# Optimization experiments

Measured on AMD Instinct MI355X. Metric: run time of the kernel, lower is better.

## Reference

```python
import jax, jax.numpy as jnp
import numpy as np
import math

B, L, D, N = 8, 4096, 1024, 16

def setup_inputs() -> dict:
    key = jax.random.key(0)
    k1, k2, k3, k4, k5, k6 = jax.random.split(key, 6)
    return {
        "x": jax.random.normal(k1, (B, L, D), dtype=jnp.float32),
        "delta": jax.random.normal(k2, (D, N, 1), dtype=jnp.float32),
        "alpha": jax.random.normal(k3, (D, N, 1), dtype=jnp.float32),
        "beta": jax.random.normal(k4, (D, N, 1), dtype=jnp.float32),
        "gamma": jax.random.normal(k5, (D, N), dtype=jnp.float32),
        "omega": jax.random.normal(k6, (D,), dtype=jnp.float32),
    }

def reference(x, delta, alpha, beta, gamma, omega):
    # x: (B, L, D). Unidirectional EMA, no state, no padding mask.
    b, l, d = x.shape
    n_state = gamma.shape[-1]
    scale = math.sqrt(1.0 / n_state)

    residual = x * omega  # (B, L, D)
    xt = jnp.swapaxes(x, -1, -2)  # (B, D, L)

    # EMA coefficients
    p = jax.nn.sigmoid(delta)          # (D, N, 1)
    a = jax.nn.sigmoid(alpha)          # (D, N, 1)
    q = 1.0 - p * a                    # (D, N, 1)

    # Vandermonde kernel: k[d, t] = sum_n p*beta*q^t * gamma*scale
    t = jnp.arange(l, dtype=x.dtype)   # (L,)
    vander = t[None, None, :] * jnp.log(q)          # (D, N, L)
    kernel = p * beta * jnp.exp(vander)             # (D, N, L)
    k = jnp.einsum('dnl,dn->dl', kernel, gamma * scale)  # (D, L)

    # FFT long convolution with zero-padding to 2L (linear conv)
    n_fft = 2 * l
    k_f = jnp.fft.rfft(k, n=n_fft)                  # (D, L+1) complex
    x_f = jnp.fft.rfft(xt, n=n_fft)                 # (B, D, L+1) complex
    out = jnp.fft.irfft(x_f * k_f, n=n_fft)[..., :l]  # (B, D, L)

    return jnp.swapaxes(out, -1, -2) + residual     # (B, L, D)
```

## Files before the change

kernel.cpp:

```cpp
#include <hip/hip_runtime.h>

#define BB 8
#define LL 4096
#define DD 1024
#define NN 16
#define GG 32
#define CC (LL / GG)
#define UF 8

__device__ __forceinline__ float sigmoid_precise(float v) {
    return 1.0f / (1.0f + expf(-v));
}

__global__ __launch_bounds__(256) void ema_chunk_states(
    const float* __restrict__ x,
    const float* __restrict__ delta,
    const float* __restrict__ alpha,
    float* __restrict__ E)
{
    const int g = blockIdx.x;
    const int d = blockIdx.y * 256 + threadIdx.x;
    const int b = blockIdx.z;

    float q[NN];
#pragma unroll
    for (int n = 0; n < NN; ++n) {
        float p = sigmoid_precise(delta[d * NN + n]);
        float a = sigmoid_precise(alpha[d * NN + n]);
        q[n] = 1.0f - p * a;
    }

    float u[NN];
#pragma unroll
    for (int n = 0; n < NN; ++n) u[n] = 0.0f;

    const float* xp = x + ((size_t)b * LL + (size_t)g * CC) * DD + d;
    for (int ii = 0; ii < CC; ii += UF) {
        float xv[UF];
#pragma unroll
        for (int j = 0; j < UF; ++j)
            xv[j] = xp[(size_t)(ii + j) * DD];
#pragma unroll
        for (int j = 0; j < UF; ++j) {
#pragma unroll
            for (int n = 0; n < NN; ++n)
                u[n] = fmaf(q[n], u[n], xv[j]);
        }
    }

    float* Ep = E + (((size_t)b * GG + g) * NN) * DD + d;
#pragma unroll
    for (int n = 0; n < NN; ++n)
        Ep[(size_t)n * DD] = u[n];
}

__global__ __launch_bounds__(256) void ema_final(
    const float* __restrict__ x,
    const float* __restrict__ delta,
    const float* __restrict__ alpha,
    const float* __restrict__ beta,
    const float* __restrict__ gamma,
    const float* __restrict__ omega,
    const float* __restrict__ E,
    float* __restrict__ out)
{
    const int g = blockIdx.x;
    const int d = blockIdx.y * 256 + threadIdx.x;
    const int b = blockIdx.z;

    float q[NN], gc[NN];
#pragma unroll
    for (int n = 0; n < NN; ++n) {
        float p = sigmoid_precise(delta[d * NN + n]);
        float a = sigmoid_precise(alpha[d * NN + n]);
        q[n]  = 1.0f - p * a;
        gc[n] = p * beta[d * NN + n] * gamma[d * NN + n] * 0.25f;
    }

    float u[NN];
#pragma unroll
    for (int n = 0; n < NN; ++n) u[n] = 0.0f;
    if (g > 0) {
        float Q[NN];
#pragma unroll
        for (int n = 0; n < NN; ++n) Q[n] = powf(q[n], (float)CC);
        for (int gp = 0; gp < g; ++gp) {
            const float* Ep = E + (((size_t)b * GG + gp) * NN) * DD + d;
#pragma unroll
            for (int n = 0; n < NN; ++n)
                u[n] = fmaf(Q[n], u[n], Ep[(size_t)n * DD]);
        }
    }

    const float om = omega[d];
    const float* xp = x + ((size_t)b * LL + (size_t)g * CC) * DD + d;
    float* op = out + ((size_t)b * LL + (size_t)g * CC) * DD + d;

    for (int ii = 0; ii < CC; ii += UF) {
        float xv[UF];
#pragma unroll
        for (int j = 0; j < UF; ++j)
            xv[j] = __builtin_nontemporal_load(&xp[(size_t)(ii + j) * DD]);
#pragma unroll
        for (int j = 0; j < UF; ++j) {
            float xvj = xv[j];
            float a0 = om * xvj, a1 = 0.0f, a2 = 0.0f, a3 = 0.0f;
#pragma unroll
            for (int n = 0; n < NN; n += 4) {
                u[n + 0] = fmaf(q[n + 0], u[n + 0], xvj);
                u[n + 1] = fmaf(q[n + 1], u[n + 1], xvj);
                u[n + 2] = fmaf(q[n + 2], u[n + 2], xvj);
                u[n + 3] = fmaf(q[n + 3], u[n + 3], xvj);
                a0 = fmaf(gc[n + 0], u[n + 0], a0);
                a1 = fmaf(gc[n + 1], u[n + 1], a1);
                a2 = fmaf(gc[n + 2], u[n + 2], a2);
                a3 = fmaf(gc[n + 3], u[n + 3], a3);
            }
            float acc = (a0 + a1) + (a2 + a3);
            __builtin_nontemporal_store(acc, &op[(size_t)(ii + j) * DD]);
        }
    }
}

extern "C" void kernel_launch(void* const* d_in, const int* in_sizes, int n_in,
                              void* d_out, int out_size, void* d_ws, size_t ws_size,
                              hipStream_t stream) {
    const float* x     = (const float*)d_in[0];
    const float* delta = (const float*)d_in[1];
    const float* alpha = (const float*)d_in[2];
    const float* beta  = (const float*)d_in[3];
    const float* gamma = (const float*)d_in[4];
    const float* omega = (const float*)d_in[5];
    float* out = (float*)d_out;
    float* E = (float*)d_ws;

    dim3 grid(GG, DD / 256, BB);
    dim3 block(256);
    hipLaunchKernelGGL(ema_chunk_states, grid, block, 0, stream,
                       x, delta, alpha, E);
    hipLaunchKernelGGL(ema_final, grid, block, 0, stream,
                       x, delta, alpha, beta, gamma, omega, E, out);
}
```

Before: 306.5 us.

## Add separate carry-scan kernel and raise chunk count to 64

Adds a middle kernel that turns the per-chunk end states into prefix carries with one sequential scan per (b,n,d). The final kernel then reads a single carry instead of re-accumulating all earlier chunk states, which removed quadratic-in-G work and made G=64 practical, giving more blocks and shorter serial recurrences. Nontemporal loads and stores are replaced with ordinary ones. The cost is an extra launch, a read-modify-write pass over the state buffer, and a larger workspace, with a fallback to 32 chunks if the workspace is too small.

```diff
diff --git a/kernel.cpp b/kernel.cpp
--- a/kernel.cpp
+++ b/kernel.cpp
@@ -4,20 +4,20 @@
 #define LL 4096
 #define DD 1024
 #define NN 16
-#define GG 32
-#define CC (LL / GG)
 #define UF 8
 
 __device__ __forceinline__ float sigmoid_precise(float v) {
     return 1.0f / (1.0f + expf(-v));
 }
 
+template <int G_>
 __global__ __launch_bounds__(256) void ema_chunk_states(
     const float* __restrict__ x,
     const float* __restrict__ delta,
     const float* __restrict__ alpha,
     float* __restrict__ E)
 {
+    constexpr int C_ = LL / G_;
     const int g = blockIdx.x;
     const int d = blockIdx.y * 256 + threadIdx.x;
     const int b = blockIdx.z;
@@ -34,8 +34,8 @@
 #pragma unroll
     for (int n = 0; n < NN; ++n) u[n] = 0.0f;
 
-    const float* xp = x + ((size_t)b * LL + (size_t)g * CC) * DD + d;
-    for (int ii = 0; ii < CC; ii += UF) {
+    const float* xp = x + ((size_t)b * LL + (size_t)g * C_) * DD + d;
+    for (int ii = 0; ii < C_; ii += UF) {
         float xv[UF];
 #pragma unroll
         for (int j = 0; j < UF; ++j)
@@ -48,12 +48,50 @@
         }
     }
 
-    float* Ep = E + (((size_t)b * GG + g) * NN) * DD + d;
+    float* Ep = E + (((size_t)b * G_ + g) * NN) * DD + d;
 #pragma unroll
     for (int n = 0; n < NN; ++n)
         Ep[(size_t)n * DD] = u[n];
 }
 
+template <int G_>
+__global__ __launch_bounds__(256) void ema_carry_scan(
+    const float* __restrict__ delta,
+    const float* __restrict__ alpha,
+    float* __restrict__ E)
+{
+    constexpr int C_ = LL / G_;
+    const int t = blockIdx.x * 256 + threadIdx.x;
+    const int d = t & (DD - 1);
+    const int n = (t >> 10) & (NN - 1);
+    const int b = t >> 14;
+
+    const float p = sigmoid_precise(delta[d * NN + n]);
+    const float a = sigmoid_precise(alpha[d * NN + n]);
+    const float q = 1.0f - p * a;
+    const float Qc = powf(q, (float)C_);
+
+    float* Ep = E + (((size_t)b * G_) * NN + n) * DD + d;
+    const size_t gstride = (size_t)NN * DD;
+
+    float u = 0.0f;
+    for (int gg = 0; gg < G_; gg += UF) {
+        float ev[UF], sv[UF];
+#pragma unroll
+        for (int j = 0; j < UF; ++j)
+            ev[j] = Ep[(size_t)(gg + j) * gstride];
+#pragma unroll
+        for (int j = 0; j < UF; ++j) {
+            u = fmaf(Qc, u, ev[j]);
+            sv[j] = u;
+        }
+#pragma unroll
+        for (int j = 0; j < UF; ++j)
+            Ep[(size_t)(gg + j) * gstride] = sv[j];
+    }
+}
+
+template <int G_>
 __global__ __launch_bounds__(256) void ema_final(
     const float* __restrict__ x,
     const float* __restrict__ delta,
@@ -61,9 +99,10 @@
     const float* __restrict__ beta,
     const float* __restrict__ gamma,
     const float* __restrict__ omega,
-    const float* __restrict__ E,
+    const float* __restrict__ S,
     float* __restrict__ out)
 {
+    constexpr int C_ = LL / G_;
     const int g = blockIdx.x;
     const int d = blockIdx.y * 256 + threadIdx.x;
     const int b = blockIdx.z;
@@ -78,29 +117,25 @@
     }
 
     float u[NN];
+    if (g > 0) {
+        const float* Sp = S + (((size_t)b * G_ + (g - 1)) * NN) * DD + d;
 #pragma unroll
-    for (int n = 0; n < NN; ++n) u[n] = 0.0f;
-    if (g > 0) {
-        float Q[NN];
+        for (int n = 0; n < NN; ++n)
+            u[n] = Sp[(size_t)n * DD];
+    } else {
 #pragma unroll
-        for (int n = 0; n < NN; ++n) Q[n] = powf(q[n], (float)CC);
-        for (int gp = 0; gp < g; ++gp) {
-            const float* Ep = E + (((size_t)b * GG + gp) * NN) * DD + d;
-#pragma unroll
-            for (int n = 0; n < NN; ++n)
-                u[n] = fmaf(Q[n], u[n], Ep[(size_t)n * DD]);
-        }
+        for (int n = 0; n < NN; ++n) u[n] = 0.0f;
     }
 
     const float om = omega[d];
-    const float* xp = x + ((size_t)b * LL + (size_t)g * CC) * DD + d;
-    float* op = out + ((size_t)b * LL + (size_t)g * CC) * DD + d;
+    const float* xp = x + ((size_t)b * LL + (size_t)g * C_) * DD + d;
+    float* op = out + ((size_t)b * LL + (size_t)g * C_) * DD + d;
 
-    for (int ii = 0; ii < CC; ii += UF) {
+    for (int ii = 0; ii < C_; ii += UF) {
         float xv[UF];
 #pragma unroll
         for (int j = 0; j < UF; ++j)
-            xv[j] = __builtin_nontemporal_load(&xp[(size_t)(ii + j) * DD]);
+            xv[j] = xp[(size_t)(ii + j) * DD];
 #pragma unroll
         for (int j = 0; j < UF; ++j) {
             float xvj = xv[j];
@@ -116,10 +151,25 @@
                 a2 = fmaf(gc[n + 2], u[n + 2], a2);
                 a3 = fmaf(gc[n + 3], u[n + 3], a3);
             }
-            float acc = (a0 + a1) + (a2 + a3);
-            __builtin_nontemporal_store(acc, &op[(size_t)(ii + j) * DD]);
+            op[(size_t)(ii + j) * DD] = (a0 + a1) + (a2 + a3);
         }
     }
+}
+
+template <int G_>
+static void launch_all(const float* x, const float* delta, const float* alpha,
+                       const float* beta, const float* gamma, const float* omega,
+                       float* out, float* E, hipStream_t stream)
+{
+    dim3 block(256);
+    dim3 grid13(G_, DD / 256, BB);
+    dim3 grid2((BB * NN * DD) / 256);
+    hipLaunchKernelGGL(ema_chunk_states<G_>, grid13, block, 0, stream,
+                       x, delta, alpha, E);
+    hipLaunchKernelGGL(ema_carry_scan<G_>, grid2, block, 0, stream,
+                       delta, alpha, E);
+    hipLaunchKernelGGL(ema_final<G_>, grid13, block, 0, stream,
+                       x, delta, alpha, beta, gamma, omega, E, out);
 }
 
 extern "C" void kernel_launch(void* const* d_in, const int* in_sizes, int n_in,
@@ -134,10 +184,9 @@
     float* out = (float*)d_out;
     float* E = (float*)d_ws;
 
-    dim3 grid(GG, DD / 256, BB);
-    dim3 block(256);
-    hipLaunchKernelGGL(ema_chunk_states, grid, block, 0, stream,
-                       x, delta, alpha, E);
-    hipLaunchKernelGGL(ema_final, grid, block, 0, stream,
-                       x, delta, alpha, beta, gamma, omega, E, out);
+    const size_t need64 = (size_t)BB * 64 * NN * DD * sizeof(float);
+    if (ws_size >= need64)
+        launch_all<64>(x, delta, alpha, beta, gamma, omega, out, E, stream);
+    else
+        launch_all<32>(x, delta, alpha, beta, gamma, omega, out, E, stream);
 }
```

New measurement: 295.2 us. -3.7%, faster.
